# Optimization experiments

Measured on AMD Instinct MI355X. Metric: run time of the kernel, lower is better.

## Reference

```python
import jax, jax.numpy as jnp
import numpy as np
import math

THRESHOLD = 0.9
CAPACITY_FACTOR = 1.0
ALPHA = 0.01


def setup_inputs() -> dict:
    key = jax.random.key(0)
    k1, k2 = jax.random.split(key)
    B, T, H, E = 8, 4096, 1024, 64
    x = jax.random.normal(k1, (B, T, H), dtype=jnp.float32)
    # kaiming-uniform-ish gate init: bound = 1/sqrt(H)
    gate_w = jax.random.uniform(k2, (E, H), dtype=jnp.float32,
                                minval=-1.0 / math.sqrt(H), maxval=1.0 / math.sqrt(H))
    return {"x": x, "gate_w": gate_w}


def reference(x, gate_w):
    B, T, H = x.shape
    E = gate_w.shape[0]
    N = B * T
    x_flat = x.reshape(N, H)

    logits = x_flat @ gate_w.T                      # [N, E]
    probs = jax.nn.softmax(logits, axis=-1)

    # per-token descending sort of expert probs
    idx_sorted = jnp.argsort(-probs, axis=-1)       # [N, E]
    p_sorted = jnp.take_along_axis(probs, idx_sorted, axis=-1)

    # variable-k threshold selection on cumulative prob
    csum = jnp.cumsum(p_sorted, axis=-1)
    reached = csum >= THRESHOLD
    reached = reached.at[:, -1].set(True)
    k_idx = jnp.argmax(reached, axis=-1)            # first True per row
    arangeE = jnp.arange(E)[None, :]
    assign_sorted = arangeE <= k_idx[:, None]       # prefix-select in sorted order

    # scatter back to expert order via inverse permutation
    inv_perm = jnp.argsort(idx_sorted, axis=-1)
    assign_mask = jnp.take_along_axis(assign_sorted, inv_perm, axis=-1)

    # priority score R: prob minus rank, -1e9 for unassigned
    rank = jnp.arange(1, E + 1, dtype=probs.dtype)[None, :]
    R_sorted = jnp.where(assign_sorted, p_sorted - rank, jnp.float32(-1e9))
    R = jnp.take_along_axis(R_sorted, inv_perm, axis=-1)  # [N, E]

    # capacity-based dropping: keep top-C tokens per expert column
    capacity = int(math.ceil(N / E) * CAPACITY_FACTOR)
    C = min(capacity, N)
    tok_sorted = jnp.argsort(-R, axis=0)            # [N, E]
    topC_tok = tok_sorted[:C, :]                    # [C, E]
    cols = jnp.broadcast_to(jnp.arange(E)[None, :], topC_tok.shape)
    keep_flags = jnp.zeros((N, E), dtype=bool).at[topC_tok, cols].set(True)

    final_mask = assign_mask & keep_flags
    scores_sel = jnp.where(final_mask, probs, jnp.zeros_like(probs))

    # aux load-balance loss on top-1 assignments
    top1_idx = jnp.argmax(probs, axis=-1)
    top1_scores = jnp.max(probs, axis=-1)
    fi = jnp.mean(jax.nn.one_hot(top1_idx, E, dtype=probs.dtype), axis=0)
    pi = jax.ops.segment_sum(top1_scores, top1_idx, num_segments=E) / jnp.float32(N)
    aux_loss = E * jnp.sum(fi * pi) * ALPHA

    return final_mask, scores_sel, aux_loss, top1_idx
```

## Files before the change

kernel.cpp:

```cpp
#include <hip/hip_runtime.h>
#include <math.h>

#define NTOK 32768
#define HDIM 1024
#define NEXP 64
#define NE   (NTOK * NEXP)
#define CAP  512
#define TB   32
#define CK   64
#define XRS  68
#define CAND 6144
#define QMAX 2048

__device__ __forceinline__ unsigned f2key(float f) {
  unsigned u = __float_as_uint(f);
  return (u & 0x80000000u) ? ~u : (u | 0x80000000u);
}
__device__ __forceinline__ int bin_of(unsigned k) {
  if (k & 0x80000000u) return 0;
  float f = __uint_as_float(~k);
  f = fminf(f, 64.5f);
  return (int)f;
}

__global__ void init_kernel(unsigned* cnt, float* sumP, unsigned* ghist) {
  int i = blockIdx.x * 256 + threadIdx.x;
  if (i < NEXP) { cnt[i] = 0u; sumP[i] = 0.f; }
  if (i < NEXP * NEXP) ghist[i] = 0u;
}

__global__ __launch_bounds__(256) void router_kernel(
    const float* __restrict__ x, const float* __restrict__ w,
    float* __restrict__ probs, unsigned* __restrict__ keyNE,
    unsigned* __restrict__ keyEN, unsigned long long* __restrict__ assignB,
    unsigned* __restrict__ cnt, float* __restrict__ sumP,
    unsigned* __restrict__ ghist, float* __restrict__ out) {
  __shared__ float sm[(TB + NEXP) * XRS];
  __shared__ unsigned lhist[NEXP * 17];
  const int tid  = threadIdx.x;
  const int wid  = tid >> 6, lane = tid & 63;
  const int tokv = wid >> 1, expv = wid & 1;
  const int tg   = lane >> 3, eg = lane & 7;
  const int t0   = blockIdx.x * TB;
  float* xs  = sm;
  float* wsm = sm + TB * XRS;

  for (int i = tid; i < NEXP * 17; i += 256) lhist[i] = 0u;

  float acc[2][4] = {};

  for (int hc = 0; hc < HDIM / CK; ++hc) {
    const int h0 = hc * CK;
#pragma unroll
    for (int r = 0; r < 2; ++r) {
      int idx = tid + r * 256;
      int row = idx >> 4, c4 = idx & 15;
      *(float4*)(xs + row * XRS + c4 * 4) =
          *(const float4*)(x + (size_t)(t0 + row) * HDIM + h0 + c4 * 4);
    }
#pragma unroll
    for (int r = 0; r < 4; ++r) {
      int idx = tid + r * 256;
      int row = idx >> 4, c4 = idx & 15;
      *(float4*)(wsm + row * XRS + c4 * 4) =
          *(const float4*)(w + (size_t)row * HDIM + h0 + c4 * 4);
    }
    __syncthreads();
#pragma unroll
    for (int s = 0; s < 16; ++s) {
      const int k4 = s * 4;
      float4 xv0 = *(const float4*)(xs + (tokv * 16 + tg) * XRS + k4);
      float4 xv1 = *(const float4*)(xs + (tokv * 16 + 8 + tg) * XRS + k4);
#pragma unroll
      for (int j = 0; j < 4; ++j) {
        float4 wv = *(const float4*)(wsm + (expv * 32 + j * 8 + eg) * XRS + k4);
        acc[0][j] += xv0.x * wv.x + xv0.y * wv.y + xv0.z * wv.z + xv0.w * wv.w;
        acc[1][j] += xv1.x * wv.x + xv1.y * wv.y + xv1.z * wv.z + xv1.w * wv.w;
      }
    }
    __syncthreads();
  }

  float* ls = sm;
  unsigned* kt = (unsigned*)(sm + TB * 65);
#pragma unroll
  for (int i = 0; i < 2; ++i) {
    int tl = tokv * 16 + i * 8 + tg;
#pragma unroll
    for (int j = 0; j < 4; ++j)
      ls[tl * 65 + expv * 32 + j * 8 + eg] = acc[i][j];
  }
  __syncthreads();

  for (int i = 0; i < 8; i += 2) {
    const int tlA = wid * 8 + i, tlB = tlA + 1;
    const int tA  = t0 + tlA,  tB  = t0 + tlB;
    float lA = ls[tlA * 65 + lane];
    float lB = ls[tlB * 65 + lane];
    float mxA = lA, mxB = lB;
#pragma unroll
    for (int m = 32; m >= 1; m >>= 1) {
      mxA = fmaxf(mxA, __shfl_xor(mxA, m));
      mxB = fmaxf(mxB, __shfl_xor(mxB, m));
    }
    float exA = expf(lA - mxA), exB = expf(lB - mxB);
    float ssA = exA, ssB = exB;
#pragma unroll
    for (int m = 32; m >= 1; m >>= 1) {
      ssA += __shfl_xor(ssA, m);
      ssB += __shfl_xor(ssB, m);
    }
    float pA = exA / ssA, pB = exB / ssB;
    int rkA = 0, rkB = 0; float csA = pA, csB = pB;
#pragma unroll
    for (int d = 1; d < 64; ++d) {
      float pjA = __shfl_xor(pA, d);
      float pjB = __shfl_xor(pB, d);
      int H = d; H |= H >> 1; H |= H >> 2; H |= H >> 4; H -= (H >> 1);
      bool jlt = (lane & H) != 0;
      bool gA = (pjA > pA) || (pjA == pA && jlt);
      bool gB = (pjB > pB) || (pjB == pB && jlt);
      rkA += gA ? 1 : 0; csA += gA ? pjA : 0.f;
      rkB += gB ? 1 : 0; csB += gB ? pjB : 0.f;
    }
    int kcA = (csA >= 0.9f) ? rkA : 63;
    int kcB = (csB >= 0.9f) ? rkB : 63;
#pragma unroll
    for (int m = 32; m >= 1; m >>= 1) {
      kcA = min(kcA, __shfl_xor(kcA, m));
      kcB = min(kcB, __shfl_xor(kcB, m));
    }
    const bool asA = (rkA <= kcA);
    const bool asB = (rkB <= kcB);
    float RA = asA ? (pA - (float)(rkA + 1)) : -1e9f;
    float RB = asB ? (pB - (float)(rkB + 1)) : -1e9f;
    unsigned keyA = f2key(RA), keyB = f2key(RB);
    probs[(size_t)tA * NEXP + lane] = pA;
    probs[(size_t)tB * NEXP + lane] = pB;
    keyNE[(size_t)tA * NEXP + lane] = keyA;
    keyNE[(size_t)tB * NEXP + lane] = keyB;
    kt[tlA * 65 + lane] = keyA;
    kt[tlB * 65 + lane] = keyB;
    {
      int bA = bin_of(keyA);
      atomicAdd(&lhist[lane * 17 + (bA >> 2)], 1u << ((bA & 3) * 8));
      int bB = bin_of(keyB);
      atomicAdd(&lhist[lane * 17 + (bB >> 2)], 1u << ((bB & 3) * 8));
    }
    unsigned long long abA = __ballot(asA);
    unsigned long long abB = __ballot(asB);
    if (lane == 0) { assignB[tA] = abA; assignB[tB] = abB; }
    if (rkA == 0) {
      out[(size_t)2 * NE + 1 + tA] = (float)lane;
      atomicAdd(&cnt[lane], 1u);
      atomicAdd(&sumP[lane], pA);
    }
    if (rkB == 0) {
      out[(size_t)2 * NE + 1 + tB] = (float)lane;
      atomicAdd(&cnt[lane], 1u);
      atomicAdd(&sumP[lane], pB);
    }
  }
  __syncthreads();
#pragma unroll
  for (int r = 0; r < 8; ++r) {
    int idx = tid + r * 256;
    int e = idx >> 5, tl = idx & 31;
    keyEN[(size_t)e * NTOK + t0 + tl] = kt[tl * 65 + e];
  }
  for (int idx = tid; idx < NEXP * NEXP; idx += 256) {
    int ee = idx >> 6, b = idx & 63;
    unsigned v = (lhist[ee * 17 + (b >> 2)] >> ((b & 3) * 8)) & 0xffu;
    if (v) atomicAdd(&ghist[idx], v);
  }
}

__global__ __launch_bounds__(1024) void select_kernel(
    const unsigned* __restrict__ keyEN, const unsigned* __restrict__ ghist,
    unsigned* __restrict__ theta, int* __restrict__ tieCut) {
  const int e = blockIdx.x;
  const unsigned* col = keyEN + (size_t)e * NTOK;
  const int tid = threadIdx.x, wid = tid >> 6;
  __shared__ unsigned wh[16][256];
  __shared__ unsigned h[256];
  __shared__ unsigned cA_k[CAND], cA_t[CAND], cB_k[CAND], cB_t[CAND];
  __shared__ unsigned s_n, s_b;
  __shared__ int s_rb, s_need, s_cnt;
  __shared__ unsigned s_theta; __shared__ int s_cut;

  if (tid == 0) {
    unsigned run = 0; int rb = -1, need = 0, cc = 0;
    for (int r = 0; r < 64; ++r) {
      unsigned c = ghist[e * 64 + r];
      if (rb < 0 && run + c >= CAP) { rb = r; need = CAP - (int)run; cc = (int)c; }
      run += c;
    }
    s_rb = rb; s_need = need; s_cnt = cc;
  }
  __syncthreads();
  if (s_rb < 0) {
    if (tid == 0) { theta[e] = f2key(-1e9f); tieCut[e] = -1; }
    return;
  }
  const int rb = s_rb;
  int need = s_need, cnt = s_cnt;
  unsigned pmask = 0u, pval = 0u;
  int level = 0;

  while (cnt > CAND && level < 4) {
    const int sh = 24 - 8 * level;
    for (int r = tid; r < 16 * 256; r += 1024) ((unsigned*)wh)[r] = 0u;
    __syncthreads();
    for (int t = tid; t < NTOK; t += 1024) {
      unsigned k = col[t];
      if (bin_of(k) == rb && (k & pmask) == pval)
        atomicAdd(&wh[wid][(k >> sh) & 255u], 1u);
    }
    __syncthreads();
    if (tid < 256) {
      unsigned s = 0;
      for (int wv = 0; wv < 16; ++wv) s += wh[wv][tid];
      h[tid] = s;
    }
    __syncthreads();
    if (tid == 0) {
      unsigned cum = 0;
      for (int d = 255; d >= 0; --d) {
        if (cum + h[d] >= (unsigned)need) {
          s_b = (unsigned)d; s_need = need - (int)cum; s_cnt = (int)h[d];
          break;
        }
        cum += h[d];
      }
    }
    __syncthreads();
    need = s_need; cnt = s_cnt;
    pmask |= (255u << sh); pval |= (s_b << sh);
    level++;
    __syncthreads();
  }

  if (cnt > CAND) {
    int lo = 0, hi = NTOK - 1;
    while (lo < hi) {
      int mid = (lo + hi) >> 1;
      if (tid == 0) s_n = 0u;
      __syncthreads();
      for (int t = tid; t <= mid; t += 1024)
        if (col[t] == pval) atomicAdd(&s_n, 1u);
      __syncthreads();
      if ((int)s_n >= need) hi = mid; else lo = mid + 1;
      __syncthreads();
    }
    if (tid == 0) { theta[e] = pval; tieCut[e] = lo; }
    return;
  }

  if (tid == 0) s_n = 0u;
  __syncthreads();
  for (int t = tid; t < NTOK; t += 1024) {
    unsigned k = col[t];
    if (bin_of(k) == rb && (k & pmask) == pval) {
      unsigned i = atomicAdd(&s_n, 1u);
      cA_k[i] = k; cA_t[i] = (unsigned)t;
    }
  }
  __syncthreads();
  unsigned* ck = cA_k; unsigned* ct = cA_t;
  unsigned* nk = cB_k; unsigned* nt2 = cB_t;

  while (cnt > QMAX && level < 4) {
    const int sh = 24 - 8 * level;
    for (int r = tid; r < 16 * 256; r += 1024) ((unsigned*)wh)[r] = 0u;
    __syncthreads();
    for (int i = tid; i < cnt; i += 1024)
      atomicAdd(&wh[wid][(ck[i] >> sh) & 255u], 1u);
    __syncthreads();
    if (tid < 256) {
      unsigned s = 0;
      for (int wv = 0; wv < 16; ++wv) s += wh[wv][tid];
      h[tid] = s;
    }
    __syncthreads();
    if (tid == 0) {
      unsigned cum = 0;
      for (int d = 255; d >= 0; --d) {
        if (cum + h[d] >= (unsigned)need) {
          s_b = (unsigned)d; s_need = need - (int)cum; s_cnt = (int)h[d];
          break;
        }
        cum += h[d];
      }
      s_n = 0u;
    }
    __syncthreads();
    for (int i = tid; i < cnt; i += 1024) {
      if (((ck[i] >> sh) & 255u) == s_b) {
        unsigned j = atomicAdd(&s_n, 1u);
        nk[j] = ck[i]; nt2[j] = ct[i];
      }
    }
    __syncthreads();
    { unsigned* t1 = ck; ck = nk; nk = t1; t1 = ct; ct = nt2; nt2 = t1; }
    need = s_need; cnt = s_cnt; level++;
    __syncthreads();
  }

  for (int i = tid; i < cnt; i += 1024) {
    unsigned ki = ck[i], ti = ct[i];
    int c = 0;
    for (int j = 0; j < cnt; ++j) {
      unsigned kj = ck[j], tj = ct[j];
      c += (kj > ki || (kj == ki && tj < ti)) ? 1 : 0;
    }
    if (c == need - 1) { s_theta = ki; s_cut = (int)ti; }
  }
  __syncthreads();
  if (tid == 0) { theta[e] = s_theta; tieCut[e] = s_cut; }
}

__global__ __launch_bounds__(256) void write_kernel(
    const float* __restrict__ probs, const unsigned* __restrict__ keyNE,
    const unsigned long long* __restrict__ assignB,
    const unsigned* __restrict__ theta, const int* __restrict__ tieCut,
    const unsigned* __restrict__ cnt, const float* __restrict__ sumP,
    float* __restrict__ out) {
  const int id = blockIdx.x * 256 + threadIdx.x;
  const int t = id >> 6, e = id & 63;
  unsigned k = keyNE[id];
  float p = probs[id];
  bool a = (assignB[t] >> e) & 1ull;
  unsigned th = theta[e];
  int cut = tieCut[e];
  bool keep = (k > th) || ((k == th) && (t <= cut));
  bool msk = a && keep;
  out[id] = msk ? 1.f : 0.f;
  out[(size_t)NE + id] = msk ? p : 0.f;
  if (blockIdx.x == 0 && threadIdx.x < 64) {
    int ee = threadIdx.x;
    float v = ((float)cnt[ee] / (float)NTOK) * (sumP[ee] / (float)NTOK);
#pragma unroll
    for (int m = 32; m >= 1; m >>= 1) v += __shfl_xor(v, m);
    if (ee == 0) out[(size_t)2 * NE] = (float)NEXP * v * 0.01f;
  }
}

extern "C" void kernel_launch(void* const* d_in, const int* in_sizes, int n_in,
                              void* d_out, int out_size, void* d_ws, size_t ws_size,
                              hipStream_t stream) {
  const float* x = (const float*)d_in[0];
  const float* w = (const float*)d_in[1];
  float* out = (float*)d_out;

  char* ws = (char*)d_ws;
  float* probs                 = (float*)ws;
  unsigned* keyNE              = (unsigned*)(probs + NE);
  unsigned* keyEN              = keyNE + NE;
  unsigned long long* assignB  = (unsigned long long*)(keyEN + NE);
  unsigned* cnt                = (unsigned*)(assignB + NTOK);
  float* sumP                  = (float*)(cnt + NEXP);
  unsigned* theta              = (unsigned*)(sumP + NEXP);
  int* tieCut                  = (int*)(theta + NEXP);
  unsigned* ghist              = (unsigned*)(tieCut + NEXP);

  init_kernel<<<16, 256, 0, stream>>>(cnt, sumP, ghist);
  router_kernel<<<NTOK / TB, 256, 0, stream>>>(x, w, probs, keyNE, keyEN,
                                               assignB, cnt, sumP, ghist, out);
  select_kernel<<<NEXP, 1024, 0, stream>>>(keyEN, ghist, theta, tieCut);
  write_kernel<<<NE / 256, 256, 0, stream>>>(probs, keyNE, assignB, theta,
                                             tieCut, cnt, sumP, out);
}
```

Baseline: 537.9 us.

## Compute router logits with split-bf16 MFMA instead of scalar fp32 FMAs

The gate GEMM now runs on bf16 MFMA instructions. Each fp32 value is split into high and low bf16 parts, and three products (hi*hi, hi*lo, lo*hi) are summed to get close to fp32 accuracy. Gate weights are split once in init_kernel and stored in the workspace. Activations are split on the fly while being staged into shared memory. This replaces the VALU-bound dot-product loop, but the dropped lo*lo term and the different rounding could flip argsort or threshold decisions on near-tied probabilities.

Measured after the change: 484.2 us. 1.11x faster.

```diff
diff --git a/kernel.cpp b/kernel.cpp
--- a/kernel.cpp
+++ b/kernel.cpp
@@ -7,10 +7,12 @@
 #define NE   (NTOK * NEXP)
 #define CAP  512
 #define TB   32
-#define CK   64
-#define XRS  68
+#define XST  80
 #define CAND 6144
 #define QMAX 2048
+
+typedef float f32x4 __attribute__((ext_vector_type(4)));
+typedef short bf16x8 __attribute__((ext_vector_type(8)));
 
 __device__ __forceinline__ unsigned f2key(float f) {
   unsigned u = __float_as_uint(f);
@@ -23,72 +25,104 @@
   return (int)f;
 }
 
-__global__ void init_kernel(unsigned* cnt, float* sumP, unsigned* ghist) {
+__device__ __forceinline__ void split_bf16(float x, short& hi, short& lo) {
+  unsigned u = __float_as_uint(x);
+  hi = (short)(u >> 16);
+  float hf = __uint_as_float(u & 0xFFFF0000u);
+  float l = x - hf;
+  lo = (short)(__float_as_uint(l) >> 16);
+}
+
+__global__ void init_kernel(unsigned* cnt, float* sumP, unsigned* ghist,
+                            const float* __restrict__ w,
+                            short* __restrict__ whi, short* __restrict__ wlo) {
   int i = blockIdx.x * 256 + threadIdx.x;
   if (i < NEXP) { cnt[i] = 0u; sumP[i] = 0.f; }
   if (i < NEXP * NEXP) ghist[i] = 0u;
+  for (int j = i; j < NEXP * HDIM; j += 4096) {
+    short h, l; split_bf16(w[j], h, l);
+    whi[j] = h; wlo[j] = l;
+  }
 }
 
 __global__ __launch_bounds__(256) void router_kernel(
-    const float* __restrict__ x, const float* __restrict__ w,
+    const float* __restrict__ x, const short* __restrict__ whig,
+    const short* __restrict__ wlog,
     float* __restrict__ probs, unsigned* __restrict__ keyNE,
     unsigned* __restrict__ keyEN, unsigned long long* __restrict__ assignB,
     unsigned* __restrict__ cnt, float* __restrict__ sumP,
     unsigned* __restrict__ ghist, float* __restrict__ out) {
-  __shared__ float sm[(TB + NEXP) * XRS];
+  __shared__ int smemi[7680];
   __shared__ unsigned lhist[NEXP * 17];
+  short* xh = (short*)smemi;
+  short* xl = xh + 32 * XST;
+  short* wh = xl + 32 * XST;
+  short* wl = wh + 64 * XST;
   const int tid  = threadIdx.x;
   const int wid  = tid >> 6, lane = tid & 63;
-  const int tokv = wid >> 1, expv = wid & 1;
-  const int tg   = lane >> 3, eg = lane & 7;
+  const int mh   = wid >> 1, nh = wid & 1;
   const int t0   = blockIdx.x * TB;
-  float* xs  = sm;
-  float* wsm = sm + TB * XRS;
 
   for (int i = tid; i < NEXP * 17; i += 256) lhist[i] = 0u;
 
-  float acc[2][4] = {};
-
-  for (int hc = 0; hc < HDIM / CK; ++hc) {
-    const int h0 = hc * CK;
-#pragma unroll
-    for (int r = 0; r < 2; ++r) {
-      int idx = tid + r * 256;
-      int row = idx >> 4, c4 = idx & 15;
-      *(float4*)(xs + row * XRS + c4 * 4) =
-          *(const float4*)(x + (size_t)(t0 + row) * HDIM + h0 + c4 * 4);
-    }
-#pragma unroll
-    for (int r = 0; r < 4; ++r) {
-      int idx = tid + r * 256;
-      int row = idx >> 4, c4 = idx & 15;
-      *(float4*)(wsm + row * XRS + c4 * 4) =
-          *(const float4*)(w + (size_t)row * HDIM + h0 + c4 * 4);
-    }
-    __syncthreads();
-#pragma unroll
-    for (int s = 0; s < 16; ++s) {
-      const int k4 = s * 4;
-      float4 xv0 = *(const float4*)(xs + (tokv * 16 + tg) * XRS + k4);
-      float4 xv1 = *(const float4*)(xs + (tokv * 16 + 8 + tg) * XRS + k4);
-#pragma unroll
-      for (int j = 0; j < 4; ++j) {
-        float4 wv = *(const float4*)(wsm + (expv * 32 + j * 8 + eg) * XRS + k4);
-        acc[0][j] += xv0.x * wv.x + xv0.y * wv.y + xv0.z * wv.z + xv0.w * wv.w;
-        acc[1][j] += xv1.x * wv.x + xv1.y * wv.y + xv1.z * wv.z + xv1.w * wv.w;
-      }
-    }
-    __syncthreads();
-  }
-
-  float* ls = sm;
-  unsigned* kt = (unsigned*)(sm + TB * 65);
-#pragma unroll
-  for (int i = 0; i < 2; ++i) {
-    int tl = tokv * 16 + i * 8 + tg;
-#pragma unroll
-    for (int j = 0; j < 4; ++j)
-      ls[tl * 65 + expv * 32 + j * 8 + eg] = acc[i][j];
+  f32x4 acc0 = {0.f, 0.f, 0.f, 0.f};
+  f32x4 acc1 = {0.f, 0.f, 0.f, 0.f};
+
+  const int xrow = tid >> 3, xk8 = (tid & 7) * 8;
+  const int wrow = tid >> 2, wk16 = (tid & 3) * 16;
+
+  for (int hc = 0; hc < HDIM / 64; ++hc) {
+    const int h0 = hc * 64;
+    {
+      const float* xp = x + (size_t)(t0 + xrow) * HDIM + h0 + xk8;
+      float4 v0 = *(const float4*)xp;
+      float4 v1 = *(const float4*)(xp + 4);
+      float f[8] = {v0.x, v0.y, v0.z, v0.w, v1.x, v1.y, v1.z, v1.w};
+      bf16x8 vh, vl;
+#pragma unroll
+      for (int j = 0; j < 8; ++j) { short h, l; split_bf16(f[j], h, l); vh[j] = h; vl[j] = l; }
+      *(bf16x8*)(xh + xrow * XST + xk8) = vh;
+      *(bf16x8*)(xl + xrow * XST + xk8) = vl;
+    }
+    {
+      const bf16x8* gh = (const bf16x8*)(whig + (size_t)wrow * HDIM + h0 + wk16);
+      const bf16x8* gl = (const bf16x8*)(wlog + (size_t)wrow * HDIM + h0 + wk16);
+      bf16x8 a = gh[0], b = gh[1], c = gl[0], d = gl[1];
+      *(bf16x8*)(wh + wrow * XST + wk16)     = a;
+      *(bf16x8*)(wh + wrow * XST + wk16 + 8) = b;
+      *(bf16x8*)(wl + wrow * XST + wk16)     = c;
+      *(bf16x8*)(wl + wrow * XST + wk16 + 8) = d;
+    }
+    __syncthreads();
+#pragma unroll
+    for (int ks = 0; ks < 2; ++ks) {
+      const int kb = ks * 32 + (lane >> 4) * 8;
+      const int ar = mh * 16 + (lane & 15);
+      const int br = nh * 32 + (lane & 15);
+      bf16x8 ah = *(const bf16x8*)(xh + ar * XST + kb);
+      bf16x8 al = *(const bf16x8*)(xl + ar * XST + kb);
+      bf16x8 bh0 = *(const bf16x8*)(wh + br * XST + kb);
+      bf16x8 bl0 = *(const bf16x8*)(wl + br * XST + kb);
+      bf16x8 bh1 = *(const bf16x8*)(wh + (br + 16) * XST + kb);
+      bf16x8 bl1 = *(const bf16x8*)(wl + (br + 16) * XST + kb);
+      acc0 = __builtin_amdgcn_mfma_f32_16x16x32_bf16(ah, bh0, acc0, 0, 0, 0);
+      acc0 = __builtin_amdgcn_mfma_f32_16x16x32_bf16(ah, bl0, acc0, 0, 0, 0);
+      acc0 = __builtin_amdgcn_mfma_f32_16x16x32_bf16(al, bh0, acc0, 0, 0, 0);
+      acc1 = __builtin_amdgcn_mfma_f32_16x16x32_bf16(ah, bh1, acc1, 0, 0, 0);
+      acc1 = __builtin_amdgcn_mfma_f32_16x16x32_bf16(ah, bl1, acc1, 0, 0, 0);
+      acc1 = __builtin_amdgcn_mfma_f32_16x16x32_bf16(al, bh1, acc1, 0, 0, 0);
+    }
+    __syncthreads();
+  }
+
+  float* ls = (float*)smemi;
+  unsigned* kt = (unsigned*)smemi + TB * 65;
+#pragma unroll
+  for (int r = 0; r < 4; ++r) {
+    int tl = mh * 16 + (lane >> 4) * 4 + r;
+    int e0 = nh * 32 + (lane & 15);
+    ls[tl * 65 + e0]      = acc0[r];
+    ls[tl * 65 + e0 + 16] = acc1[r];
   }
   __syncthreads();
 
@@ -362,10 +396,13 @@
   unsigned* theta              = (unsigned*)(sumP + NEXP);
   int* tieCut                  = (int*)(theta + NEXP);
   unsigned* ghist              = (unsigned*)(tieCut + NEXP);
-
-  init_kernel<<<16, 256, 0, stream>>>(cnt, sumP, ghist);
-  router_kernel<<<NTOK / TB, 256, 0, stream>>>(x, w, probs, keyNE, keyEN,
-                                               assignB, cnt, sumP, ghist, out);
+  short* whi                   = (short*)(ghist + NEXP * NEXP);
+  short* wlo                   = whi + NEXP * HDIM;
+
+  init_kernel<<<16, 256, 0, stream>>>(cnt, sumP, ghist, w, whi, wlo);
+  router_kernel<<<NTOK / TB, 256, 0, stream>>>(x, whi, wlo, probs, keyNE,
+                                               keyEN, assignB, cnt, sumP,
+                                               ghist, out);
   select_kernel<<<NEXP, 1024, 0, stream>>>(keyEN, ghist, theta, tieCut);
   write_kernel<<<NE / 256, 256, 0, stream>>>(probs, keyNE, assignB, theta,
                                              tieCut, cnt, sumP, out);
```
